# Kernel optimization log

Hardware: AMD Instinct MI355X
Metric: run time of the kernel (lower is better)

## Reference

```python
import jax, jax.numpy as jnp
import numpy as np

B, L, M, H = 16, 1024, 1024, 128
NEG = -1e30


def setup_inputs() -> dict:
    key = jax.random.key(0)
    ks = jax.random.split(key, 8)
    return {
        "text": jax.random.normal(ks[0], (B, L, H), dtype=jnp.float32),
        "modality": jax.random.normal(ks[1], (B, M, H), dtype=jnp.float32),
        "text_mask": jax.random.randint(ks[2], (B, L), 0, 2, dtype=jnp.int32),
        "modality_mask": jax.random.randint(ks[3], (B, M), 0, 2, dtype=jnp.int32),
        # learned parameters (xavier-uniform style scale)
        "text_weight": jax.random.normal(ks[4], (H, 1), dtype=jnp.float32) * 0.1,
        "modality_weight": jax.random.normal(ks[5], (H, 1), dtype=jnp.float32) * 0.1,
        "text_modality_weight": jax.random.normal(ks[6], (1, 1, H), dtype=jnp.float32) * 0.1,
        "bias": jnp.zeros((1,), dtype=jnp.float32),
    }


def reference(text, modality, text_mask, modality_mask,
              text_weight, modality_weight, text_modality_weight, bias):
    # similarity matrix s: (B, L, M)   (eval mode: dropout is identity)
    s0 = jnp.matmul(text, text_weight)                      # (B, L, 1)
    s1 = jnp.swapaxes(jnp.matmul(modality, modality_weight), 1, 2)  # (B, 1, M)
    s2 = jnp.einsum('blh,bmh->blm', text * text_modality_weight, modality)
    s = s0 + s1 + s2 + bias                                 # (B, L, M)

    mmask = modality_mask[:, None, :].astype(jnp.float32)   # (B, 1, M)
    tmask = text_mask[:, :, None].astype(jnp.float32)       # (B, L, 1)
    p1 = jax.nn.softmax(mmask * s + (1.0 - mmask) * NEG, axis=2)  # text->modality
    p2 = jax.nn.softmax(tmask * s + (1.0 - tmask) * NEG, axis=1)  # modality->text

    a = jnp.matmul(p1, modality)                            # (B, L, H)
    b = jnp.matmul(jnp.matmul(p1, jnp.swapaxes(p2, 1, 2)), text)  # (B, L, H)
    return jnp.concatenate([text, a, text * a, text * b], axis=2)  # (B, L, 8H)
```

## Files before the change

kernel.cpp:

```cpp
#include <hip/hip_runtime.h>

#define B_ 16
#define L_ 1024
#define M_ 1024
#define H_ 128

typedef unsigned short u16;
typedef unsigned int u32;
typedef __bf16 bf16x8 __attribute__((ext_vector_type(8)));
typedef float f32x4 __attribute__((ext_vector_type(4)));

__device__ __forceinline__ u16 f2bf(float x){
  u32 u = __float_as_uint(x);
  u = (u + 0x7fffu + ((u >> 16) & 1u)) >> 16;
  return (u16)u;
}

__global__ __launch_bounds__(256) void zero_f32(float4* __restrict__ p, int n4)
{
  int i = blockIdx.x * 256 + threadIdx.x;
  int stride = gridDim.x * 256;
  for (; i < n4; i += stride) p[i] = make_float4(0.f, 0.f, 0.f, 0.f);
}

__global__ __launch_bounds__(256) void prep2(
    const float* __restrict__ text, const float* __restrict__ modality,
    const int* __restrict__ tmask, const int* __restrict__ mmask,
    const float* __restrict__ tw, const float* __restrict__ mw,
    const float* __restrict__ tmw,
    u16* __restrict__ textw_bf, u16* __restrict__ mod_bf,
    u16* __restrict__ textT_bf, u16* __restrict__ modT_bf,
    float* __restrict__ t0, float* __restrict__ s1m)
{
  int g = blockIdx.x;
  int sel = g >> 8;
  int b = (g >> 4) & 15;
  int r0 = (g & 15) * 64;
  const float* src = (sel ? modality : text) + ((size_t)b * 1024 + r0) * H_;
  const int* msk = (sel ? mmask : tmask) + b * 1024 + r0;
  const float* dotw = sel ? mw : tw;
  u16* rowout = (sel ? mod_bf : textw_bf) + ((size_t)b * 1024 + r0) * H_;
  u16* trout = (sel ? modT_bf : textT_bf) + (size_t)b * H_ * 1024 + r0;
  float* dotout = (sel ? s1m : t0) + b * 1024 + r0;

  __shared__ u16 tile[128][72];
  int tid = threadIdx.x;
  int rgrp = tid >> 5;
  int lane32 = tid & 31;
  int h0 = lane32 * 4;
  float4 w4 = *(const float4*)&dotw[h0];
  float4 mv = sel ? make_float4(1.f, 1.f, 1.f, 1.f) : *(const float4*)&tmw[h0];
  float dpart[8];
  #pragma unroll
  for (int p = 0; p < 8; p++) {
    int row = rgrp + p * 8;
    float4 x = *(const float4*)&src[(size_t)row * H_ + h0];
    dpart[p] = x.x * w4.x + x.y * w4.y + x.z * w4.z + x.w * w4.w;
    uint2 pk;
    pk.x = (u32)f2bf(x.x * mv.x) | ((u32)f2bf(x.y * mv.y) << 16);
    pk.y = (u32)f2bf(x.z * mv.z) | ((u32)f2bf(x.w * mv.w) << 16);
    *(uint2*)&rowout[(size_t)row * H_ + h0] = pk;
    int mk = msk[row];
    tile[h0 + 0][row] = mk ? f2bf(x.x) : (u16)0;
    tile[h0 + 1][row] = mk ? f2bf(x.y) : (u16)0;
    tile[h0 + 2][row] = mk ? f2bf(x.z) : (u16)0;
    tile[h0 + 3][row] = mk ? f2bf(x.w) : (u16)0;
  }
  #pragma unroll
  for (int p = 0; p < 8; p++) {
    float d = dpart[p];
    #pragma unroll
    for (int off = 1; off < 32; off <<= 1) d += __shfl_xor(d, off);
    if (lane32 == 0) dotout[rgrp + p * 8] = d;
  }
  __syncthreads();
  int lcol = (tid & 7) * 8;
  #pragma unroll
  for (int p = 0; p < 4; p++) {
    int h = (tid >> 3) + p * 32;
    uint4 v = *(const uint4*)&tile[h][lcol];
    *(uint4*)&trout[(size_t)h * 1024 + lcol] = v;
  }
}

__global__ __launch_bounds__(256) void gemm_exp(
    const u16* __restrict__ A, const u16* __restrict__ Bm,
    const float* __restrict__ t0, const float* __restrict__ s1m,
    const float* __restrict__ bias, const int* __restrict__ tmask,
    const int* __restrict__ mmask, float* __restrict__ rowsum,
    float* __restrict__ colsum, u16* __restrict__ ET)
{
  int f = blockIdx.x;
  int orig = (f & 7) * 256 + (f >> 3);
  int b = orig >> 7;
  int a0 = (orig & 15) * 64, b0 = ((orig >> 4) & 7) * 128;
  int tid = threadIdx.x, lane = tid & 63, wid = tid >> 6;
  int wr = wid >> 1, wc = wid & 1;
  int c = lane & 15, q = lane >> 4;
  __shared__ __align__(16) char smem[24576];
  const u16* Ab = A + (size_t)(b * L_ + a0) * H_;
  const u16* Bb = Bm + (size_t)(b * M_ + b0) * H_;
  f32x4 acc[2][4];
  #pragma unroll
  for (int i = 0; i < 2; i++)
    #pragma unroll
    for (int j = 0; j < 4; j++) acc[i][j] = (f32x4){0.f, 0.f, 0.f, 0.f};
  for (int kt = 0; kt < 2; kt++) {
    __syncthreads();
    #pragma unroll
    for (int i = 0; i < 2; i++) {
      int cc = tid + 256 * i;
      int row = cc >> 3, col8 = cc & 7;
      uint4 v = *(const uint4*)(Ab + (size_t)row * H_ + kt * 64 + col8 * 8);
      *(uint4*)(smem + row * 128 + ((col8 * 16) ^ ((row & 7) << 4))) = v;
    }
    #pragma unroll
    for (int i = 0; i < 4; i++) {
      int cc = tid + 256 * i;
      int row = cc >> 3, col8 = cc & 7;
      uint4 v = *(const uint4*)(Bb + (size_t)row * H_ + kt * 64 + col8 * 8);
      *(uint4*)(smem + 8192 + row * 128 + ((col8 * 16) ^ ((row & 7) << 4))) = v;
    }
    __syncthreads();
    #pragma unroll
    for (int kk = 0; kk < 2; kk++) {
      int kbyte = kk * 64 + (q << 4);
      bf16x8 af[2], bfr[4];
      #pragma unroll
      for (int i = 0; i < 2; i++) {
        int ra = wr * 32 + i * 16 + c;
        af[i] = *(const bf16x8*)(smem + ra * 128 + (kbyte ^ ((ra & 7) << 4)));
      }
      #pragma unroll
      for (int j = 0; j < 4; j++) {
        int rb = wc * 64 + j * 16 + c;
        bfr[j] = *(const bf16x8*)(smem + 8192 + rb * 128 + (kbyte ^ ((rb & 7) << 4)));
      }
      #pragma unroll
      for (int i = 0; i < 2; i++)
        #pragma unroll
        for (int j = 0; j < 4; j++)
          acc[i][j] = __builtin_amdgcn_mfma_f32_16x16x32_bf16(af[i], bfr[j], acc[i][j], 0, 0, 0);
    }
  }
  float biasv = bias[0];
  float t0v[2][4];
  int tmv[2][4];
  #pragma unroll
  for (int i = 0; i < 2; i++)
    #pragma unroll
    for (int r = 0; r < 4; r++) {
      int ar = a0 + wr * 32 + i * 16 + q * 4 + r;
      t0v[i][r] = t0[b * L_ + ar];
      tmv[i][r] = tmask[b * L_ + ar];
    }
  float s1v[4];
  int mmv[4];
  #pragma unroll
  for (int j = 0; j < 4; j++) {
    int gcol = b0 + wc * 64 + j * 16 + c;
    s1v[j] = s1m[b * M_ + gcol];
    mmv[j] = mmask[b * M_ + gcol];
  }
  float ev[2][4][4];
  #pragma unroll
  for (int i = 0; i < 2; i++)
    #pragma unroll
    for (int j = 0; j < 4; j++)
      #pragma unroll
      for (int r = 0; r < 4; r++)
        ev[i][j][r] = __expf(acc[i][j][r] + t0v[i][r] + s1v[j] + biasv);
  #pragma unroll
  for (int i = 0; i < 2; i++)
    #pragma unroll
    for (int r = 0; r < 4; r++) {
      float prs = 0.f;
      #pragma unroll
      for (int j = 0; j < 4; j++) prs += mmv[j] ? ev[i][j][r] : 0.f;
      #pragma unroll
      for (int off = 1; off < 16; off <<= 1) prs += __shfl_xor(prs, off);
      if (c == 0) {
        int ar = a0 + wr * 32 + i * 16 + q * 4 + r;
        atomicAdd(&rowsum[b * L_ + ar], prs);
      }
    }
  #pragma unroll
  for (int j = 0; j < 4; j++) {
    float pcs = 0.f;
    #pragma unroll
    for (int i = 0; i < 2; i++)
      #pragma unroll
      for (int r = 0; r < 4; r++) pcs += tmv[i][r] ? ev[i][j][r] : 0.f;
    pcs += __shfl_xor(pcs, 16);
    pcs += __shfl_xor(pcs, 32);
    if (q == 0) {
      int gcol = b0 + wc * 64 + j * 16 + c;
      atomicAdd(&colsum[b * M_ + gcol], pcs);
    }
  }
  __syncthreads();
  u16* et = (u16*)smem;
  #pragma unroll
  for (int i = 0; i < 2; i++)
    #pragma unroll
    for (int j = 0; j < 4; j++) {
      int gcolL = wc * 64 + j * 16 + c;
      int arL = wr * 32 + i * 16 + q * 4;
      u32 lo = (u32)f2bf(ev[i][j][0]) | ((u32)f2bf(ev[i][j][1]) << 16);
      u32 hi = (u32)f2bf(ev[i][j][2]) | ((u32)f2bf(ev[i][j][3]) << 16);
      uint2 pk; pk.x = lo; pk.y = hi;
      *(uint2*)&et[gcolL * 72 + arL] = pk;
    }
  __syncthreads();
  #pragma unroll
  for (int it = 0; it < 4; it++) {
    int mrow = (tid >> 3) + it * 32;
    int l8 = tid & 7;
    uint4 v = *(const uint4*)&et[mrow * 72 + l8 * 8];
    *(uint4*)&ET[((size_t)(b * M_ + b0 + mrow)) * L_ + a0 + l8 * 8] = v;
  }
}

__global__ __launch_bounds__(512) void gemm_ct(
    const u16* __restrict__ A, const u16* __restrict__ ET,
    float* __restrict__ c_f32)
{
  int f = blockIdx.x;
  int orig = (f & 7) * 64 + (f >> 3);
  int b = orig >> 5;
  int x = orig & 3, y = (orig >> 2) & 7;
  int ia = x & 1, ks = x >> 1;
  int a0 = ia * 64, b0 = y * 128;
  int tid = threadIdx.x, lane = tid & 63, wid = tid >> 6;
  int wr = wid >> 2, wc = wid & 3;
  int c = lane & 15, q = lane >> 4;
  __shared__ __align__(16) char smem[24576];
  const u16* Ab = A + (size_t)(b * H_ + a0) * L_;
  const u16* Bb = ET + (size_t)(b * M_ + b0) * L_;
  f32x4 acc[2][2];
  #pragma unroll
  for (int i = 0; i < 2; i++)
    #pragma unroll
    for (int j = 0; j < 2; j++) acc[i][j] = (f32x4){0.f, 0.f, 0.f, 0.f};
  for (int kt = ks * 8; kt < ks * 8 + 8; kt++) {
    __syncthreads();
    {
      int row = tid >> 3, col8 = tid & 7;
      uint4 v = *(const uint4*)(Ab + (size_t)row * L_ + kt * 64 + col8 * 8);
      *(uint4*)(smem + row * 128 + ((col8 * 16) ^ ((row & 7) << 4))) = v;
    }
    #pragma unroll
    for (int i = 0; i < 2; i++) {
      int cc = tid + 512 * i;
      int row = cc >> 3, col8 = cc & 7;
      uint4 v = *(const uint4*)(Bb + (size_t)row * L_ + kt * 64 + col8 * 8);
      *(uint4*)(smem + 8192 + row * 128 + ((col8 * 16) ^ ((row & 7) << 4))) = v;
    }
    __syncthreads();
    #pragma unroll
    for (int kk = 0; kk < 2; kk++) {
      int kbyte = kk * 64 + (q << 4);
      bf16x8 af[2], bfr[2];
      #pragma unroll
      for (int i = 0; i < 2; i++) {
        int ra = wr * 32 + i * 16 + c;
        af[i] = *(const bf16x8*)(smem + ra * 128 + (kbyte ^ ((ra & 7) << 4)));
      }
      #pragma unroll
      for (int j = 0; j < 2; j++) {
        int rb = wc * 32 + j * 16 + c;
        bfr[j] = *(const bf16x8*)(smem + 8192 + rb * 128 + (kbyte ^ ((rb & 7) << 4)));
      }
      #pragma unroll
      for (int i = 0; i < 2; i++)
        #pragma unroll
        for (int j = 0; j < 2; j++)
          acc[i][j] = __builtin_amdgcn_mfma_f32_16x16x32_bf16(af[i], bfr[j], acc[i][j], 0, 0, 0);
    }
  }
  #pragma unroll
  for (int i = 0; i < 2; i++)
    #pragma unroll
    for (int j = 0; j < 2; j++) {
      int arow0 = a0 + wr * 32 + i * 16 + q * 4;
      int gcol = b0 + wc * 32 + j * 16 + c;
      #pragma unroll
      for (int r = 0; r < 4; r++)
        atomicAdd(&c_f32[((size_t)(b * H_ + arow0 + r)) * M_ + gcol], acc[i][j][r]);
    }
}

__global__ __launch_bounds__(1024) void gemm_ab(
    const u16* __restrict__ ET, const u16* __restrict__ B1,
    const float* __restrict__ c_f32, const float* __restrict__ colsum,
    const int* __restrict__ mmask, const float* __restrict__ rowsum,
    const float* __restrict__ text, float* __restrict__ out)
{
  int f = blockIdx.x;
  int orig = (f & 7) * 32 + (f >> 3);
  int b = orig >> 4;
  int a0 = (orig & 15) * 64;
  int tid = threadIdx.x, lane = tid & 63, wid = tid >> 6;
  int wr = wid >> 3, wc = wid & 7;
  int c = lane & 15, q = lane >> 4;
  __shared__ __align__(16) u16 At[64 * 76];
  __shared__ __align__(16) char Bs[2][16384];
  __shared__ float invcm[1024];
  const u16* ETb = ET + (size_t)b * M_ * L_;
  const u16* B1b = B1 + (size_t)b * H_ * M_;
  const float* cfb = c_f32 + (size_t)b * H_ * M_;
  invcm[tid] = mmask[b * M_ + tid] ? 1.0f / fmaxf(colsum[b * M_ + tid], 1e-30f) : 0.f;

  int sArow = tid >> 4, sAcol = (tid & 15) * 4;
  int sBrow = tid >> 3, sBcol8 = tid & 7;

  f32x4 acc_a[2], acc_b[2];
  #pragma unroll
  for (int i = 0; i < 2; i++) {
    acc_a[i] = (f32x4){0.f, 0.f, 0.f, 0.f};
    acc_b[i] = (f32x4){0.f, 0.f, 0.f, 0.f};
  }

  uint2 rA;
  uint4 rB1;
  float4 rB2a, rB2b;
  auto LOAD = [&](int kt) {
    rA = *(const uint2*)&ETb[((size_t)(kt * 64 + sArow)) * L_ + a0 + sAcol];
    int mbase = kt * 64 + sBcol8 * 8;
    rB1 = *(const uint4*)(B1b + (size_t)sBrow * M_ + mbase);
    rB2a = *(const float4*)&cfb[(size_t)sBrow * M_ + mbase];
    rB2b = *(const float4*)&cfb[(size_t)sBrow * M_ + mbase + 4];
  };
  auto WRITE = [&](int kt) {
    *(uint2*)(At + sArow * 76 + sAcol) = rA;
    int swz = (sBcol8 * 16) ^ ((sBrow & 7) << 4);
    *(uint4*)(Bs[0] + sBrow * 128 + swz) = rB1;
    int mbase = kt * 64 + sBcol8 * 8;
    float4 ia4 = *(const float4*)&invcm[mbase];
    float4 ib4 = *(const float4*)&invcm[mbase + 4];
    uint4 v2;
    v2.x = (u32)f2bf(rB2a.x * ia4.x) | ((u32)f2bf(rB2a.y * ia4.y) << 16);
    v2.y = (u32)f2bf(rB2a.z * ia4.z) | ((u32)f2bf(rB2a.w * ia4.w) << 16);
    v2.z = (u32)f2bf(rB2b.x * ib4.x) | ((u32)f2bf(rB2b.y * ib4.y) << 16);
    v2.w = (u32)f2bf(rB2b.z * ib4.z) | ((u32)f2bf(rB2b.w * ib4.w) << 16);
    *(uint4*)(Bs[1] + sBrow * 128 + swz) = v2;
  };

  LOAD(0);
  __syncthreads();
  WRITE(0);
  for (int kt = 0; kt < 16; kt++) {
    if (kt < 15) LOAD(kt + 1);
    __syncthreads();
    #pragma unroll
    for (int kk = 0; kk < 2; kk++) {
      int kbyte = kk * 64 + (q << 4);
      bf16x8 af[2], b1f, b2f;
      #pragma unroll
      for (int i = 0; i < 2; i++) {
        int lidx = wr * 32 + i * 16 + c;
        int mbase = kk * 32 + q * 8;
        union { unsigned short s[8]; bf16x8 v; } ua;
        #pragma unroll
        for (int e = 0; e < 8; e++) ua.s[e] = At[(mbase + e) * 76 + lidx];
        af[i] = ua.v;
      }
      int rb = wc * 16 + c;
      b1f = *(const bf16x8*)(Bs[0] + rb * 128 + (kbyte ^ ((rb & 7) << 4)));
      b2f = *(const bf16x8*)(Bs[1] + rb * 128 + (kbyte ^ ((rb & 7) << 4)));
      #pragma unroll
      for (int i = 0; i < 2; i++) {
        acc_a[i] = __builtin_amdgcn_mfma_f32_16x16x32_bf16(af[i], b1f, acc_a[i], 0, 0, 0);
        acc_b[i] = __builtin_amdgcn_mfma_f32_16x16x32_bf16(af[i], b2f, acc_b[i], 0, 0, 0);
      }
    }
    __syncthreads();
    if (kt < 15) WRITE(kt + 1);
  }

  float irs[2][4];
  #pragma unroll
  for (int i = 0; i < 2; i++)
    #pragma unroll
    for (int r = 0; r < 4; r++) {
      int ar = a0 + wr * 32 + i * 16 + q * 4 + r;
      irs[i][r] = 1.0f / fmaxf(rowsum[b * L_ + ar], 1e-30f);
    }
  int gcol = wc * 16 + c;
  #pragma unroll
  for (int i = 0; i < 2; i++) {
    #pragma unroll
    for (int r = 0; r < 4; r++) {
      int ar = a0 + wr * 32 + i * 16 + q * 4 + r;
      float av = acc_a[i][r] * irs[i][r];
      float bv = acc_b[i][r] * irs[i][r];
      float tv = text[((size_t)(b * L_ + ar)) * H_ + gcol];
      size_t base = ((size_t)(b * L_ + ar)) * 512 + gcol;
      out[base] = tv;
      out[base + 128] = av;
      out[base + 256] = tv * av;
      out[base + 384] = tv * bv;
    }
  }
}

extern "C" void kernel_launch(void* const* d_in, const int* in_sizes, int n_in,
                              void* d_out, int out_size, void* d_ws, size_t ws_size,
                              hipStream_t stream) {
  const float* text = (const float*)d_in[0];
  const float* modality = (const float*)d_in[1];
  const int* text_mask = (const int*)d_in[2];
  const int* modality_mask = (const int*)d_in[3];
  const float* text_weight = (const float*)d_in[4];
  const float* modality_weight = (const float*)d_in[5];
  const float* tmw = (const float*)d_in[6];
  const float* bias = (const float*)d_in[7];
  float* out = (float*)d_out;
  (void)in_sizes; (void)n_in; (void)out_size; (void)ws_size;

  char* ws = (char*)d_ws;
  size_t off = 0;
  auto alloc = [&](size_t bytes) { void* p = ws + off; off += (bytes + 255) & ~(size_t)255; return p; };
  u16*   ET       = (u16*)  alloc((size_t)B_ * M_ * L_ * 2);
  u16*   textw_bf = (u16*)  alloc((size_t)B_ * L_ * H_ * 2);
  u16*   mod_bf   = (u16*)  alloc((size_t)B_ * M_ * H_ * 2);
  u16*   textT_bf = (u16*)  alloc((size_t)B_ * H_ * L_ * 2);
  u16*   mod_bfT  = (u16*)  alloc((size_t)B_ * H_ * M_ * 2);
  float* t0       = (float*)alloc((size_t)B_ * L_ * 4);
  float* s1m      = (float*)alloc((size_t)B_ * M_ * 4);
  float* rowsum   = (float*)alloc((size_t)B_ * L_ * 4);
  float* colsum   = (float*)alloc((size_t)B_ * M_ * 4);
  float* c_f32    = (float*)alloc((size_t)B_ * H_ * M_ * 4);

  int n4 = (B_ * (L_ + M_) + B_ * H_ * M_) / 4;
  zero_f32<<<2048, 256, 0, stream>>>((float4*)rowsum, n4);
  prep2<<<512, 256, 0, stream>>>(text, modality, text_mask, modality_mask,
      text_weight, modality_weight, tmw,
      textw_bf, mod_bf, textT_bf, mod_bfT, t0, s1m);
  gemm_exp<<<2048, 256, 0, stream>>>(textw_bf, mod_bf, t0, s1m, bias,
      text_mask, modality_mask, rowsum, colsum, ET);
  gemm_ct<<<512, 512, 0, stream>>>(textT_bf, ET, c_f32);
  gemm_ab<<<256, 1024, 0, stream>>>(ET, mod_bfT, c_f32, colsum, modality_mask,
      rowsum, text, out);
}
```

Measured before the change: 166.0 us.

## Fuse zeroing into prep, use direct global-to-LDS loads, prefetch in gemm_ct

Folds the zero-initialisation of the accumulator buffers into the prep kernel, removing one launch. In gemm_exp the register-staged tile copies become global_load_lds direct-to-LDS loads, with the swizzle moved into the global address instead of the LDS address. In gemm_ct the next K tile is prefetched into registers during the MFMA loop and written to shared memory after a second barrier, overlapping global latency with compute. The B tile is written at a fixed offset across two 8 KB halves, so the row mapping must match the existing read indexing.

```diff
diff --git a/kernel.cpp b/kernel.cpp
--- a/kernel.cpp
+++ b/kernel.cpp
@@ -16,11 +16,10 @@
   return (u16)u;
 }
 
-__global__ __launch_bounds__(256) void zero_f32(float4* __restrict__ p, int n4)
-{
-  int i = blockIdx.x * 256 + threadIdx.x;
-  int stride = gridDim.x * 256;
-  for (; i < n4; i += stride) p[i] = make_float4(0.f, 0.f, 0.f, 0.f);
+__device__ __forceinline__ void gload16(const u16* g, char* l) {
+  __builtin_amdgcn_global_load_lds(
+      (const __attribute__((address_space(1))) u32*)(const void*)g,
+      (__attribute__((address_space(3))) u32*)(void*)l, 16, 0, 0);
 }
 
 __global__ __launch_bounds__(256) void prep2(
@@ -30,8 +29,12 @@
     const float* __restrict__ tmw,
     u16* __restrict__ textw_bf, u16* __restrict__ mod_bf,
     u16* __restrict__ textT_bf, u16* __restrict__ modT_bf,
-    float* __restrict__ t0, float* __restrict__ s1m)
+    float* __restrict__ t0, float* __restrict__ s1m,
+    float4* __restrict__ zbase, int n4)
 {
+  for (int i = blockIdx.x * 256 + threadIdx.x; i < n4; i += 512 * 256)
+    zbase[i] = make_float4(0.f, 0.f, 0.f, 0.f);
+
   int g = blockIdx.x;
   int sel = g >> 8;
   int b = (g >> 4) & 15;
@@ -100,6 +103,8 @@
   __shared__ __align__(16) char smem[24576];
   const u16* Ab = A + (size_t)(b * L_ + a0) * H_;
   const u16* Bb = Bm + (size_t)(b * M_ + b0) * H_;
+  int rsub = lane >> 3;
+  int scol8 = (lane & 7) ^ rsub;
   f32x4 acc[2][4];
   #pragma unroll
   for (int i = 0; i < 2; i++)
@@ -108,19 +113,13 @@
   for (int kt = 0; kt < 2; kt++) {
     __syncthreads();
     #pragma unroll
-    for (int i = 0; i < 2; i++) {
-      int cc = tid + 256 * i;
-      int row = cc >> 3, col8 = cc & 7;
-      uint4 v = *(const uint4*)(Ab + (size_t)row * H_ + kt * 64 + col8 * 8);
-      *(uint4*)(smem + row * 128 + ((col8 * 16) ^ ((row & 7) << 4))) = v;
-    }
-    #pragma unroll
-    for (int i = 0; i < 4; i++) {
-      int cc = tid + 256 * i;
-      int row = cc >> 3, col8 = cc & 7;
-      uint4 v = *(const uint4*)(Bb + (size_t)row * H_ + kt * 64 + col8 * 8);
-      *(uint4*)(smem + 8192 + row * 128 + ((col8 * 16) ^ ((row & 7) << 4))) = v;
-    }
+    for (int i = 0; i < 2; i++)
+      gload16(Ab + (size_t)(wid * 8 + i * 32 + rsub) * H_ + kt * 64 + scol8 * 8,
+              smem + wid * 1024 + i * 4096);
+    #pragma unroll
+    for (int i = 0; i < 4; i++)
+      gload16(Bb + (size_t)(wid * 8 + i * 32 + rsub) * H_ + kt * 64 + scol8 * 8,
+              smem + 8192 + wid * 1024 + i * 4096);
     __syncthreads();
     #pragma unroll
     for (int kk = 0; kk < 2; kk++) {
@@ -237,25 +236,30 @@
   __shared__ __align__(16) char smem[24576];
   const u16* Ab = A + (size_t)(b * H_ + a0) * L_;
   const u16* Bb = ET + (size_t)(b * M_ + b0) * L_;
+  int sRow = tid >> 3, sCol8 = tid & 7;
+  int swzA = sRow * 128 + ((sCol8 * 16) ^ ((sRow & 7) << 4));
   f32x4 acc[2][2];
   #pragma unroll
   for (int i = 0; i < 2; i++)
     #pragma unroll
     for (int j = 0; j < 2; j++) acc[i][j] = (f32x4){0.f, 0.f, 0.f, 0.f};
-  for (int kt = ks * 8; kt < ks * 8 + 8; kt++) {
-    __syncthreads();
-    {
-      int row = tid >> 3, col8 = tid & 7;
-      uint4 v = *(const uint4*)(Ab + (size_t)row * L_ + kt * 64 + col8 * 8);
-      *(uint4*)(smem + row * 128 + ((col8 * 16) ^ ((row & 7) << 4))) = v;
-    }
-    #pragma unroll
-    for (int i = 0; i < 2; i++) {
-      int cc = tid + 512 * i;
-      int row = cc >> 3, col8 = cc & 7;
-      uint4 v = *(const uint4*)(Bb + (size_t)row * L_ + kt * 64 + col8 * 8);
-      *(uint4*)(smem + 8192 + row * 128 + ((col8 * 16) ^ ((row & 7) << 4))) = v;
-    }
+
+  uint4 rA, rB0, rB1;
+  auto LOAD = [&](int kt) {
+    rA = *(const uint4*)(Ab + (size_t)sRow * L_ + kt * 64 + sCol8 * 8);
+    rB0 = *(const uint4*)(Bb + (size_t)sRow * L_ + kt * 64 + sCol8 * 8);
+    rB1 = *(const uint4*)(Bb + (size_t)(sRow + 64) * L_ + kt * 64 + sCol8 * 8);
+  };
+  auto WRITE = [&]() {
+    *(uint4*)(smem + swzA) = rA;
+    *(uint4*)(smem + 8192 + swzA) = rB0;
+    *(uint4*)(smem + 8192 + 8192 + swzA) = rB1;
+  };
+  int kt0 = ks * 8;
+  LOAD(kt0);
+  WRITE();
+  for (int t = 0; t < 8; t++) {
+    if (t < 7) LOAD(kt0 + t + 1);
     __syncthreads();
     #pragma unroll
     for (int kk = 0; kk < 2; kk++) {
@@ -277,6 +281,8 @@
         for (int j = 0; j < 2; j++)
           acc[i][j] = __builtin_amdgcn_mfma_f32_16x16x32_bf16(af[i], bfr[j], acc[i][j], 0, 0, 0);
     }
+    __syncthreads();
+    if (t < 7) WRITE();
   }
   #pragma unroll
   for (int i = 0; i < 2; i++)
@@ -433,10 +439,9 @@
   float* c_f32    = (float*)alloc((size_t)B_ * H_ * M_ * 4);
 
   int n4 = (B_ * (L_ + M_) + B_ * H_ * M_) / 4;
-  zero_f32<<<2048, 256, 0, stream>>>((float4*)rowsum, n4);
   prep2<<<512, 256, 0, stream>>>(text, modality, text_mask, modality_mask,
       text_weight, modality_weight, tmw,
-      textw_bf, mod_bf, textT_bf, mod_bfT, t0, s1m);
+      textw_bf, mod_bf, textT_bf, mod_bfT, t0, s1m, (float4*)rowsum, n4);
   gemm_exp<<<2048, 256, 0, stream>>>(textw_bf, mod_bf, t0, s1m, bias,
       text_mask, modality_mask, rowsum, colsum, ET);
   gemm_ct<<<512, 512, 0, stream>>>(textT_bf, ET, c_f32);
```

New measurement: 160.2 us. -3.5%, faster.
